# Kernel tuning notes

Measured on AMD Instinct MI355X. Metric: run time of the kernel, lower is better.

The kernel has to match this reference:

```python
import jax, jax.numpy as jnp
import numpy as np

# --- model dims ---
N = 360        # nodes
B = 8          # batch
T = 7500       # hidden_steps = tr/dt = 750/0.1
RATIO = 10     # dt_ratio = dtt/dt
HEMO = T // RATIO
INPUT = 2
DMAX = 500

# --- FastDMFParams defaults ---
DT = 0.1
SQRT_DT = DT ** 0.5
DTT_S = 1.0 / 1000.0            # dtt / 1000 (seconds)
W_E, W_I, I_0 = 1.0, 0.7, 0.382
TAU_E, TAU_I = 100.0, 10.0
GAMMA_E, GAMMA_I = 0.641 / 1000.0, 1.0 / 1000.0
SIGMA_E, SIGMA_I = 0.005, 0.005
AE, BE, DE = 310.0, 125.0, 0.16
AI, BI, DI = 615.0, 177.0, 0.087
G, JN = 2.0, 0.15
G_EE = 1.4
ITAU_S, ITAU_F, ITAU_0 = 1.0 / 0.65, 1.0 / 0.41, 1.0 / 0.98
IALPHA, RHO = 1.0 / 0.32, 0.34
K1, K2, K3 = 2.38, 2.0, 0.48
V0 = 0.2


def setup_inputs() -> dict:
    key = jax.random.key(0)
    k1, k2, k3, k4 = jax.random.split(key, 4)
    baseline = jnp.array([0.0, 0.0, 0.0, 1.0, 1.0, 1.0], jnp.float32).reshape(1, 6, 1)
    state = 0.45 * jax.random.uniform(k1, (N, 6, B), jnp.float32) + baseline
    delays = jnp.zeros((N, DMAX, B), jnp.float32)  # unused (use_delay_based=False)
    noise_in = jax.random.normal(k2, (N, T, INPUT, B), jnp.float32)
    noise_out = jax.random.normal(k3, (N, B), jnp.float32)
    sc = jax.random.uniform(k4, (B, N, N), jnp.float32) / N  # normalized structural connectivity
    return {"state": state, "delays": delays, "noise_in": noise_in,
            "noise_out": noise_out, "sc": sc}


def _firing_rate(a, b, d, cur):
    x = a * cur - b
    return x / (1.0 - jnp.exp(-d * x) + 1e-8)


def _simulate(state, noise_in, noise_out, sc):
    E, I = state[:, 0, :], state[:, 1, :]          # (N,B)
    s, f = state[:, 2, :], state[:, 3, :]
    v, q = state[:, 4, :], state[:, 5, :]

    # inhibitory gain (non-scalar branch): Ji = 1 + 0.75*g*rowsum(sc), (N,B)
    Ji = (1.0 + 0.75 * G * jnp.sum(sc, axis=-1)).T

    # (N,T,INPUT,B) -> (HEMO, RATIO, N, INPUT, B)
    noise = jnp.transpose(noise_in, (1, 0, 2, 3)).reshape(HEMO, RATIO, N, INPUT, B)

    def neural_step(carry, nz):
        E, I = carry
        En, In = nz[:, 0, :], nz[:, 1, :]
        conn = jnp.einsum('bnm,mb->nb', sc, E)                 # delayed-coupling surrogate
        I_E = jax.nn.relu(W_E * I_0 + G_EE * JN * E + G * JN * conn - Ji * I)
        I_I = jax.nn.relu(W_I * I_0 + JN * E - I)
        R_E = _firing_rate(AE, BE, DE, I_E)
        R_I = _firing_rate(AI, BI, DI, I_I)
        dE = -E / TAU_E + (1.0 - E) * GAMMA_E * R_E
        dI = -I / TAU_I + GAMMA_I * R_I
        E = jax.nn.relu(E + DT * dE + SIGMA_E * En * SQRT_DT)
        I = jax.nn.relu(I + DT * dI + SIGMA_I * In * SQRT_DT)
        return (E, I), None

    def hemo_step(carry, noise_block):
        E, I, s, f, v, q = carry
        (E, I), _ = jax.lax.scan(neural_step, (E, I), noise_block)
        # Balloon-Windkessel Euler step at dtt (seconds)
        v_ia = v ** IALPHA
        ds = E - ITAU_S * s - ITAU_F * (f - 1.0)
        df = s
        dv = (f - v_ia) * ITAU_0
        dq = (f / RHO * (1.0 - (1.0 - RHO) ** (1.0 / f)) - q * v_ia / v) * ITAU_0
        s = s + DTT_S * ds
        f = f + DTT_S * df
        v = v + DTT_S * dv
        q = q + DTT_S * dq
        return (E, I, s, f, v, q), None

    (E, I, s, f, v, q), _ = jax.lax.scan(hemo_step, (E, I, s, f, v, q), noise)
    bold = 100.0 * V0 * (K1 * (1.0 - q) + K2 * (1.0 - q / v) + K3 * (1.0 - v)) + noise_out
    next_state = jnp.stack([E, I, s, f, v, q], axis=1)  # (N,6,B)
    return next_state, bold


def reference(state, delays, noise_in, noise_out, sc):
    # delays buffer unused (params.use_delay_based = False)
    return _simulate(state, noise_in, noise_out, sc)
```

## Files before the change

### kernel.cpp

```cpp
#include <hip/hip_runtime.h>


typedef unsigned int u32;
typedef int i32x4 __attribute__((ext_vector_type(4)));

#define NN 360
#define NB 8
#define NT 7500
#define NHEMO 750

#define S_SC 45720.0f
#define S_E  64.0f
#define CONN_K 1.0252653e-7f

__device__ __forceinline__ float frcp(float x) {
#if __has_builtin(__builtin_amdgcn_rcpf)
  return __builtin_amdgcn_rcpf(x);
#else
  return 1.0f / x;
#endif
}
__device__ __forceinline__ float fexp2(float x) {
#if __has_builtin(__builtin_amdgcn_exp2f)
  return __builtin_amdgcn_exp2f(x);
#else
  return exp2f(x);
#endif
}
__device__ __forceinline__ float flog2(float x) {
#if __has_builtin(__builtin_amdgcn_logf)
  return __builtin_amdgcn_logf(x);
#else
  return log2f(x);
#endif
}

__device__ __forceinline__ void lds_barrier() {
  __builtin_amdgcn_sched_barrier(0);
  asm volatile("s_waitcnt lgkmcnt(0)" ::: "memory");
  __builtin_amdgcn_s_barrier();
  asm volatile("" ::: "memory");
  __builtin_amdgcn_sched_barrier(0);
}

__global__ __launch_bounds__(512, 2) void dmf_kernel(
    const float* __restrict__ state,
    const float* __restrict__ noise_in,
    const float* __restrict__ noise_out,
    const float* __restrict__ sc,
    float* __restrict__ out)
{
  const int b   = blockIdx.x;
  const int tid = threadIdx.x;
  const int w   = tid >> 6;
  const int l   = tid & 63;
  const int g   = l >> 4;
  const int r   = l & 15;
  const int t_o = r >> 2;
  const int j_o = r & 3;
  const int R_o = 48*w + 16*t_o + 4*g + j_o;
  const bool upd = (r < 12) && (R_o < NN);
  const int Rn  = upd ? R_o : 0;

  __shared__ u32 xq[2][96];

  if (tid < 192) ((u32*)xq)[tid] = 0;

  i32x4 afr[3][6];
  float rs[3];
  #pragma unroll
  for (int t = 0; t < 3; ++t) {
    const int R = 48*w + 16*t + r;
    const bool rv = (R < NN);
    const float* sp = sc + ((size_t)b*NN + (rv ? R : 0))*NN;
    float acc = 0.f;
    #pragma unroll
    for (int kf = 0; kf < 6; ++kf) {
      i32x4 pk;
      #pragma unroll
      for (int d = 0; d < 4; ++d) {
        int packv = 0;
        #pragma unroll
        for (int e = 0; e < 4; ++e) {
          const int k = 64*kf + 16*g + 4*d + e;
          int q = 0;
          if (rv && k < NN) {
            const float x = sp[k];
            acc += x;
            q = (int)rintf(x * S_SC);
          }
          packv |= q << (8*e);
        }
        pk[d] = packv;
      }
      afr[t][kf] = pk;
    }
    rs[t] = acc;
  }
  #pragma unroll
  for (int t = 0; t < 3; ++t) {
    rs[t] += __shfl_xor(rs[t], 16, 64);
    rs[t] += __shfl_xor(rs[t], 32, 64);
  }
  const int rho = 4*g + j_o;
  const int qs0 = __builtin_amdgcn_ds_bpermute(4*rho, __float_as_int(rs[0]));
  const int qs1 = __builtin_amdgcn_ds_bpermute(4*rho, __float_as_int(rs[1]));
  const int qs2 = __builtin_amdgcn_ds_bpermute(4*rho, __float_as_int(rs[2]));
  const float rsum = __int_as_float((t_o == 0) ? qs0 : ((t_o == 1) ? qs1 : qs2));

  float E=0.f, I=0.f, ss=0.f, ff=0.f, vv=0.f, qq=0.f, Ji=0.f;
  const float* np = noise_in + (size_t)Rn * NT * 2 * NB + b;
  float n0E=0.f, n0I=0.f, n1E=0.f, n1I=0.f;
  __syncthreads();
  if (upd) {
    Ji = 1.0f + 1.5f * rsum;
    const float* st = state + (size_t)R_o * 6 * NB + b;
    E  = st[0];
    I  = st[NB];
    ss = st[2*NB];
    ff = st[3*NB];
    vv = st[4*NB];
    qq = st[5*NB];
    int qv = (int)rintf(E * S_E);
    qv = qv > 127 ? 127 : qv;
    ((char*)&xq[0][0])[R_o] = (char)qv;
    n0E = np[0];      n0I = np[NB];
    n1E = np[2*NB];   n1I = np[3*NB];
  }
  np += 4*NB;
  __syncthreads();

  const u32* xb0 = &xq[0][4*g];
  const u32* xb1 = &xq[1][4*g];
  char* pb0 = (char*)&xq[0][0] + Rn;
  char* pb1 = (char*)&xq[1][0] + Rn;
  const bool w7 = (w == 7);

  auto body = [&](const u32* xb, char* pbn, bool PF, bool hemo) {
    i32x4 bf[6];
    #pragma unroll
    for (int kf = 0; kf < 6; ++kf) bf[kf] = *(const i32x4*)(xb + 16*kf);

    float n2E = n1E, n2I = n1I;
    if (PF) {
      if (upd) { n2E = np[0]; n2I = np[NB]; }
      np += 2*NB;
    }

    i32x4 ac0 = {0,0,0,0}, ac1 = {0,0,0,0}, ac2 = {0,0,0,0};
    #pragma unroll
    for (int kf = 0; kf < 6; ++kf)
      ac0 = __builtin_amdgcn_mfma_i32_16x16x64_i8(afr[0][kf], bf[kf], ac0, 0, 0, 0);
    #pragma unroll
    for (int kf = 0; kf < 6; ++kf)
      ac1 = __builtin_amdgcn_mfma_i32_16x16x64_i8(afr[1][kf], bf[kf], ac1, 0, 0, 0);
    if (!w7) {
      #pragma unroll
      for (int kf = 0; kf < 6; ++kf)
        ac2 = __builtin_amdgcn_mfma_i32_16x16x64_i8(afr[2][kf], bf[kf], ac2, 0, 0, 0);
    }

    const i32x4 at = (t_o == 0) ? ac0 : ((t_o == 1) ? ac1 : ac2);
    const int ci = (j_o == 0) ? at.x : ((j_o == 1) ? at.y : ((j_o == 2) ? at.z : at.w));

    if (upd) {
      const float cs = (float)ci * CONN_K;
      float I_E = fmaxf(0.382f + 0.21f*E + cs - Ji*I, 0.f);
      float I_I = fmaxf(0.2674f + 0.15f*E - I, 0.f);
      const float xE  = 310.f*I_E - 125.f;
      const float R_E = xE * frcp(1.f - fexp2(-0.23083120f*xE) + 1e-8f);
      const float xI  = 615.f*I_I - 177.f;
      const float R_I = xI * frcp(1.f - fexp2(-0.12551447f*xI) + 1e-8f);
      const float dE = -E*0.01f + (1.f - E)*0.000641f*R_E;
      const float dI = -I*0.1f  + 0.001f*R_I;
      E = fmaxf(E + 0.1f*dE + 0.00158113883f*n0E, 0.f);
      I = fmaxf(I + 0.1f*dI + 0.00158113883f*n0I, 0.f);
      int qv = (int)(E * S_E + 0.5f);
      qv = qv > 127 ? 127 : qv;
      *pbn = (char)qv;
      if (hemo) {
        const float l2v  = flog2(vv);
        const float v_ia = fexp2(3.125f * l2v);
        const float v_r  = fexp2(2.125f * l2v);
        const float ds_  = E - 1.53846153846f*ss - 2.43902439024f*(ff - 1.f);
        const float df_  = ss;
        const float dv_  = (ff - v_ia) * 1.02040816327f;
        const float pw   = fexp2(-0.59946207f * frcp(ff));
        const float dq_  = (ff*2.94117647059f*(1.f - pw) - qq*v_r) * 1.02040816327f;
        ss += 1e-3f*ds_;
        ff += 1e-3f*df_;
        vv += 1e-3f*dv_;
        qq += 1e-3f*dq_;
      }
    }
    n0E = n1E; n0I = n1I;
    n1E = n2E; n1I = n2I;
    lds_barrier();
  };

  for (int hs = 0; hs < NHEMO; ++hs) {
    body(xb0, pb1, true, false);
    body(xb1, pb0, true, false);
    body(xb0, pb1, true, false);
    body(xb1, pb0, true, false);
    body(xb0, pb1, true, false);
    body(xb1, pb0, true, false);
    body(xb0, pb1, true, false);
    body(xb1, pb0, true, false);
    if (hs != NHEMO - 1) {
      body(xb0, pb1, true, false);
      body(xb1, pb0, true, true);
    } else {
      body(xb0, pb1, false, false);
      body(xb1, pb0, false, true);
    }
  }

  if (upd) {
    float* o = out + (size_t)R_o * 6 * NB + b;
    o[0]    = E;
    o[NB]   = I;
    o[2*NB] = ss;
    o[3*NB] = ff;
    o[4*NB] = vv;
    o[5*NB] = qq;
    out[NN*6*NB + R_o*NB + b] =
        20.f*(2.38f*(1.f - qq) + 2.f*(1.f - qq/vv) + 0.48f*(1.f - vv))
        + noise_out[R_o*NB + b];
  }
}

extern "C" void kernel_launch(void* const* d_in, const int* in_sizes, int n_in,
                              void* d_out, int out_size, void* d_ws, size_t ws_size,
                              hipStream_t stream) {
  const float* state     = (const float*)d_in[0];
  const float* noise_in  = (const float*)d_in[2];
  const float* noise_out = (const float*)d_in[3];
  const float* sc        = (const float*)d_in[4];
  float* out = (float*)d_out;
  dmf_kernel<<<NB, 512, 0, stream>>>(state, noise_in, noise_out, sc, out);
}
```

Baseline: 4.388 ms.

## Split coupling matvec between MFMA waves and VALU dot4 waves

Waves 0-3 keep computing the int8 coupling product for rows 0-191 with MFMA. Waves 4-7 now handle rows 192-359 with packed int8 dot4 VALU instructions and DPP reductions across lane groups, holding their slice of the quantized connectivity in registers. The goal is to shorten the per-step critical path by spreading the matvec across both the matrix cores and the vector ALUs instead of queueing every wave on MFMA. The cost is more register pressure in the VALU waves (72 packed ints) and an uneven amount of work between the two wave groups.

```diff
diff --git a/kernel.cpp b/kernel.cpp
--- a/kernel.cpp
+++ b/kernel.cpp
@@ -12,6 +12,18 @@
 #define S_SC 45720.0f
 #define S_E  64.0f
 #define CONN_K 1.0252653e-7f
+
+#if __has_builtin(__builtin_amdgcn_sdot4)
+#define DOT4(a,b,c) __builtin_amdgcn_sdot4((a),(b),(c),false)
+#elif __has_builtin(__builtin_amdgcn_udot4)
+#define DOT4(a,b,c) (int)__builtin_amdgcn_udot4((u32)(a),(u32)(b),(u32)(c),false)
+#else
+static __device__ __forceinline__ int DOT4(int a, int b, int c) {
+  #pragma unroll
+  for (int i = 0; i < 4; ++i) c += ((a >> (8*i)) & 0xff) * ((b >> (8*i)) & 0xff);
+  return c;
+}
+#endif
 
 __device__ __forceinline__ float frcp(float x) {
 #if __has_builtin(__builtin_amdgcn_rcpf)
@@ -33,6 +45,15 @@
 #else
   return log2f(x);
 #endif
+}
+
+template <int CTRL>
+__device__ __forceinline__ int dpp_add_i(int x) {
+  return x + __builtin_amdgcn_mov_dpp(x, CTRL, 0xF, 0xF, true);
+}
+template <int CTRL>
+__device__ __forceinline__ float dpp_add_f(float x) {
+  return x + __int_as_float(__builtin_amdgcn_mov_dpp(__float_as_int(x), CTRL, 0xF, 0xF, true));
 }
 
 __device__ __forceinline__ void lds_barrier() {
@@ -54,59 +75,107 @@
   const int tid = threadIdx.x;
   const int w   = tid >> 6;
   const int l   = tid & 63;
+  const bool mcl = (w < 4);
+
   const int g   = l >> 4;
   const int r   = l & 15;
   const int t_o = r >> 2;
   const int j_o = r & 3;
-  const int R_o = 48*w + 16*t_o + 4*g + j_o;
-  const bool upd = (r < 12) && (R_o < NN);
-  const int Rn  = upd ? R_o : 0;
+  const int cg  = l & 3;
+  const int rg  = l >> 2;
+
+  int R_o; bool upd;
+  if (mcl) {
+    R_o = 48*w + 16*t_o + 4*g + j_o;
+    upd = (r < 12);
+  } else {
+    R_o = 192 + 42*(w - 4) + 3*rg + cg;
+    upd = (cg < 3) && (rg < 14);
+  }
+  const int Rn = upd ? R_o : 0;
 
   __shared__ u32 xq[2][96];
 
   if (tid < 192) ((u32*)xq)[tid] = 0;
 
   i32x4 afr[3][6];
-  float rs[3];
-  #pragma unroll
-  for (int t = 0; t < 3; ++t) {
-    const int R = 48*w + 16*t + r;
-    const bool rv = (R < NN);
-    const float* sp = sc + ((size_t)b*NN + (rv ? R : 0))*NN;
-    float acc = 0.f;
+  int   scp[3][24];
+  float rsum = 0.f;
+
+  if (mcl) {
+    float rs[3];
     #pragma unroll
-    for (int kf = 0; kf < 6; ++kf) {
-      i32x4 pk;
-      #pragma unroll
-      for (int d = 0; d < 4; ++d) {
+    for (int t = 0; t < 3; ++t) {
+      const int R = 48*w + 16*t + r;
+      const float* sp = sc + ((size_t)b*NN + R)*NN;
+      float acc = 0.f;
+      #pragma unroll
+      for (int kf = 0; kf < 6; ++kf) {
+        i32x4 pk;
+        #pragma unroll
+        for (int d = 0; d < 4; ++d) {
+          int packv = 0;
+          #pragma unroll
+          for (int e = 0; e < 4; ++e) {
+            const int k = 64*kf + 16*g + 4*d + e;
+            int q = 0;
+            if (k < NN) {
+              const float x = sp[k];
+              acc += x;
+              q = (int)rintf(x * S_SC);
+            }
+            packv |= q << (8*e);
+          }
+          pk[d] = packv;
+        }
+        afr[t][kf] = pk;
+      }
+      rs[t] = acc;
+    }
+    #pragma unroll
+    for (int t = 0; t < 3; ++t) {
+      rs[t] += __shfl_xor(rs[t], 16, 64);
+      rs[t] += __shfl_xor(rs[t], 32, 64);
+    }
+    const int rho = 4*g + j_o;
+    const int qs0 = __builtin_amdgcn_ds_bpermute(4*rho, __float_as_int(rs[0]));
+    const int qs1 = __builtin_amdgcn_ds_bpermute(4*rho, __float_as_int(rs[1]));
+    const int qs2 = __builtin_amdgcn_ds_bpermute(4*rho, __float_as_int(rs[2]));
+    rsum = __int_as_float((t_o == 0) ? qs0 : ((t_o == 1) ? qs1 : qs2));
+  } else {
+    float rs[3];
+    const int base = 192 + 42*(w - 4);
+    #pragma unroll
+    for (int j = 0; j < 3; ++j) {
+      const int rr = 3*rg + j;
+      const bool rv = (rr < 42);
+      const float* sp = sc + ((size_t)b*NN + (rv ? base + rr : 0))*NN;
+      float rsj = 0.f;
+      #pragma unroll
+      for (int k = 0; k < 24; ++k) {
         int packv = 0;
         #pragma unroll
         for (int e = 0; e < 4; ++e) {
-          const int k = 64*kf + 16*g + 4*d + e;
+          const int cc = 96*cg + 4*k + e;
           int q = 0;
-          if (rv && k < NN) {
-            const float x = sp[k];
-            acc += x;
+          if (rv && cc < NN) {
+            const float x = sp[cc];
+            rsj += x;
             q = (int)rintf(x * S_SC);
           }
           packv |= q << (8*e);
         }
-        pk[d] = packv;
+        scp[j][k] = packv;
       }
-      afr[t][kf] = pk;
-    }
-    rs[t] = acc;
-  }
-  #pragma unroll
-  for (int t = 0; t < 3; ++t) {
-    rs[t] += __shfl_xor(rs[t], 16, 64);
-    rs[t] += __shfl_xor(rs[t], 32, 64);
-  }
-  const int rho = 4*g + j_o;
-  const int qs0 = __builtin_amdgcn_ds_bpermute(4*rho, __float_as_int(rs[0]));
-  const int qs1 = __builtin_amdgcn_ds_bpermute(4*rho, __float_as_int(rs[1]));
-  const int qs2 = __builtin_amdgcn_ds_bpermute(4*rho, __float_as_int(rs[2]));
-  const float rsum = __int_as_float((t_o == 0) ? qs0 : ((t_o == 1) ? qs1 : qs2));
+      rs[j] = rsj;
+    }
+    #pragma unroll
+    for (int j = 0; j < 3; ++j) {
+      rs[j] = dpp_add_f<0xB1>(rs[j]);
+      rs[j] = dpp_add_f<0x4E>(rs[j]);
+    }
+    rsum = (cg == 0) ? rs[0] : ((cg == 1) ? rs[1] : rs[2]);
+  }
 
   float E=0.f, I=0.f, ss=0.f, ff=0.f, vv=0.f, qq=0.f, Ji=0.f;
   const float* np = noise_in + (size_t)Rn * NT * 2 * NB + b;
@@ -130,38 +199,55 @@
   np += 4*NB;
   __syncthreads();
 
-  const u32* xb0 = &xq[0][4*g];
-  const u32* xb1 = &xq[1][4*g];
+  const u32* rb0 = &xq[0][0] + (mcl ? 4*g : 24*cg);
+  const u32* rb1 = &xq[1][0] + (mcl ? 4*g : 24*cg);
   char* pb0 = (char*)&xq[0][0] + Rn;
   char* pb1 = (char*)&xq[1][0] + Rn;
-  const bool w7 = (w == 7);
-
-  auto body = [&](const u32* xb, char* pbn, bool PF, bool hemo) {
-    i32x4 bf[6];
-    #pragma unroll
-    for (int kf = 0; kf < 6; ++kf) bf[kf] = *(const i32x4*)(xb + 16*kf);
-
+
+  auto body = [&](const u32* rb, char* pbn, bool PF, bool hemo) {
     float n2E = n1E, n2I = n1I;
     if (PF) {
       if (upd) { n2E = np[0]; n2I = np[NB]; }
       np += 2*NB;
     }
 
-    i32x4 ac0 = {0,0,0,0}, ac1 = {0,0,0,0}, ac2 = {0,0,0,0};
-    #pragma unroll
-    for (int kf = 0; kf < 6; ++kf)
-      ac0 = __builtin_amdgcn_mfma_i32_16x16x64_i8(afr[0][kf], bf[kf], ac0, 0, 0, 0);
-    #pragma unroll
-    for (int kf = 0; kf < 6; ++kf)
-      ac1 = __builtin_amdgcn_mfma_i32_16x16x64_i8(afr[1][kf], bf[kf], ac1, 0, 0, 0);
-    if (!w7) {
+    int ci;
+    if (mcl) {
+      i32x4 bf[6];
+      #pragma unroll
+      for (int kf = 0; kf < 6; ++kf) bf[kf] = *(const i32x4*)(rb + 16*kf);
+      i32x4 ac0 = {0,0,0,0}, ac1 = {0,0,0,0}, ac2 = {0,0,0,0};
+      #pragma unroll
+      for (int kf = 0; kf < 6; ++kf)
+        ac0 = __builtin_amdgcn_mfma_i32_16x16x64_i8(afr[0][kf], bf[kf], ac0, 0, 0, 0);
+      #pragma unroll
+      for (int kf = 0; kf < 6; ++kf)
+        ac1 = __builtin_amdgcn_mfma_i32_16x16x64_i8(afr[1][kf], bf[kf], ac1, 0, 0, 0);
       #pragma unroll
       for (int kf = 0; kf < 6; ++kf)
         ac2 = __builtin_amdgcn_mfma_i32_16x16x64_i8(afr[2][kf], bf[kf], ac2, 0, 0, 0);
-    }
-
-    const i32x4 at = (t_o == 0) ? ac0 : ((t_o == 1) ? ac1 : ac2);
-    const int ci = (j_o == 0) ? at.x : ((j_o == 1) ? at.y : ((j_o == 2) ? at.z : at.w));
+      const i32x4 at = (t_o == 0) ? ac0 : ((t_o == 1) ? ac1 : ac2);
+      ci = (j_o == 0) ? at.x : ((j_o == 1) ? at.y : ((j_o == 2) ? at.z : at.w));
+    } else {
+      i32x4 ev4[6];
+      #pragma unroll
+      for (int kk = 0; kk < 6; ++kk) ev4[kk] = *(const i32x4*)(rb + 4*kk);
+      int a0 = 0, a1 = 0, a2 = 0;
+      #pragma unroll
+      for (int kk = 0; kk < 6; ++kk) {
+        #pragma unroll
+        for (int d = 0; d < 4; ++d) {
+          const int ex = ev4[kk][d];
+          a0 = DOT4(scp[0][4*kk + d], ex, a0);
+          a1 = DOT4(scp[1][4*kk + d], ex, a1);
+          a2 = DOT4(scp[2][4*kk + d], ex, a2);
+        }
+      }
+      a0 = dpp_add_i<0xB1>(a0); a0 = dpp_add_i<0x4E>(a0);
+      a1 = dpp_add_i<0xB1>(a1); a1 = dpp_add_i<0x4E>(a1);
+      a2 = dpp_add_i<0xB1>(a2); a2 = dpp_add_i<0x4E>(a2);
+      ci = (cg == 0) ? a0 : ((cg == 1) ? a1 : a2);
+    }
 
     if (upd) {
       const float cs = (float)ci * CONN_K;
@@ -199,20 +285,20 @@
   };
 
   for (int hs = 0; hs < NHEMO; ++hs) {
-    body(xb0, pb1, true, false);
-    body(xb1, pb0, true, false);
-    body(xb0, pb1, true, false);
-    body(xb1, pb0, true, false);
-    body(xb0, pb1, true, false);
-    body(xb1, pb0, true, false);
-    body(xb0, pb1, true, false);
-    body(xb1, pb0, true, false);
+    body(rb0, pb1, true, false);
+    body(rb1, pb0, true, false);
+    body(rb0, pb1, true, false);
+    body(rb1, pb0, true, false);
+    body(rb0, pb1, true, false);
+    body(rb1, pb0, true, false);
+    body(rb0, pb1, true, false);
+    body(rb1, pb0, true, false);
     if (hs != NHEMO - 1) {
-      body(xb0, pb1, true, false);
-      body(xb1, pb0, true, true);
+      body(rb0, pb1, true, false);
+      body(rb1, pb0, true, true);
     } else {
-      body(xb0, pb1, false, false);
-      body(xb1, pb0, false, true);
+      body(rb0, pb1, false, false);
+      body(rb1, pb0, false, true);
     }
   }
 
```

Measured after the change: 4.777 ms. 1.09x slower.
